# Kernel tuning notes

Hardware: AMD Instinct MI355X
Metric: run time of the kernel (lower is better)

The kernel has to match this reference:

```python
import jax, jax.numpy as jnp
import numpy as np

# ---- HashGrid config (tcnn defaults from module __init__) ----
N_LEVELS = 6
F = 2                      # n_features_per_level
T = 2 ** 19                # hashmap size
BASE = 16                  # base_resolution, per_level_scale=2.0
_RES = [BASE * (2 ** l) for l in range(N_LEVELS)]          # 16..512
_SIZES = [min(r ** 3, T) for r in _RES]                    # dense if grid fits
_OFFSETS = [0] + list(np.cumsum(_SIZES))
TOTAL_ENTRIES = int(_OFFSETS[-1])
_PRIMES = (1, 2654435761, 805459861)
BOX_R = 1.0
DIM_H = 64
DIM_IN = 3 + N_LEVELS * F


def hash_encode(xn, grid):
    """Multi-res hash-grid encoding. xn: [N,3] in [0,1]; grid: [TOTAL_ENTRIES, F]."""
    feats = []
    for l in range(N_LEVELS):
        res, size, off = _RES[l], _SIZES[l], _OFFSETS[l]
        dense = (res ** 3) <= T
        pos = xn * jnp.float32(res - 1) + 0.5          # tcnn: scale*x + 0.5
        pg = jnp.floor(pos)
        frac = pos - pg                                # [N,3]
        pgi = pg.astype(jnp.uint32)
        acc = jnp.zeros((xn.shape[0], F), xn.dtype)
        for corner in range(8):                        # trilinear, 8 corners
            cb = jnp.array([(corner >> d) & 1 for d in range(3)], dtype=jnp.uint32)
            c = pgi + cb                               # [N,3] corner coords
            w = jnp.prod(jnp.where(cb == 1, frac, 1.0 - frac), axis=-1)  # [N]
            if dense:
                c = jnp.minimum(c, jnp.uint32(res - 1))
                idx = c[:, 0] + c[:, 1] * jnp.uint32(res) + c[:, 2] * jnp.uint32(res * res)
            else:
                idx = ((c[:, 0] * jnp.uint32(_PRIMES[0]))
                       ^ (c[:, 1] * jnp.uint32(_PRIMES[1]))
                       ^ (c[:, 2] * jnp.uint32(_PRIMES[2]))) % jnp.uint32(size)
            acc = acc + w[:, None] * grid[jnp.uint32(off) + idx]
        feats.append(acc)
    return jnp.concatenate(feats, axis=-1)             # [N, 12]


def setup_inputs() -> dict:
    key = jax.random.key(0)
    k0, k1, k2 = jax.random.split(key, 3)
    N = 2_097_152
    x = jax.random.uniform(k0, (N, 3), jnp.float32, -1.0, 1.0)
    grid = jax.random.uniform(k1, (TOTAL_ENTRIES, F), jnp.float32, -1e-2, 1e-2)
    W0 = jax.random.normal(k2, (DIM_IN, DIM_H), jnp.float32) * float(np.sqrt(2.0 / DIM_H))
    b0 = jnp.zeros((DIM_H,), jnp.float32)
    W1 = jnp.full((DIM_H, 1), float(np.sqrt(np.pi / DIM_H)), jnp.float32)
    b1 = jnp.full((1,), -1.0, jnp.float32)             # -init_radius
    return {"x": x, "grid": grid, "W0": W0, "b0": b0, "W1": W1, "b1": b1}


def reference(x, grid, W0, b0, W1, b1):
    xn = (x + BOX_R) / (2.0 * BOX_R)                   # normalize to [0,1]
    f = hash_encode(xn, grid)                          # [N,12]
    h = jnp.concatenate([x, f], axis=-1)               # [N,15]
    h = jax.nn.relu(h @ W0 + b0)                       # [N,64]
    return h @ W1 + b1                                 # [N,1] scalar level s
```

## Files before the change

### kernel.cpp

```cpp
#include <hip/hip_runtime.h>


#define HP1 2654435761u
#define HP2 805459861u
#define HMASK ((1u << 19) - 1u)

static __device__ __forceinline__ unsigned umin_(unsigned a, unsigned b) {
    return a < b ? a : b;
}

static __device__ __forceinline__ unsigned f2bf(float f) {
    unsigned u = __float_as_uint(f);
    return (u + 0x7fffu + ((u >> 16) & 1u)) >> 16;
}
static __device__ __forceinline__ float bf2f_lo(unsigned p) {
    return __uint_as_float((p & 0xffffu) << 16);
}
static __device__ __forceinline__ float bf2f_hi(unsigned p) {
    return __uint_as_float(p & 0xffff0000u);
}

__global__ __launch_bounds__(256) void prep_kernel(
    const float* __restrict__ W0, const float* __restrict__ b0,
    const float* __restrict__ W1, const float* __restrict__ b1,
    float* __restrict__ wt)
{
    for (int t = threadIdx.x; t < 1024; t += 256) {
        const int j = t >> 4, i = t & 15;
        wt[t] = (i == 15) ? b0[j] : W0[i * 64 + j];
    }
    if (threadIdx.x < 64) wt[1024 + threadIdx.x] = W1[threadIdx.x];
    if (threadIdx.x == 0) wt[1088] = b1[0];
}

__global__ __launch_bounds__(256) void hash_level_kernel(
    const float* __restrict__ x,
    const float2* __restrict__ tab,
    unsigned* __restrict__ feat,
    float scale, int N)
{
    const int gid = blockIdx.x * 256 + threadIdx.x;
    if (gid >= N) return;

    const float px = __builtin_nontemporal_load(x + 3 * gid + 0);
    const float py = __builtin_nontemporal_load(x + 3 * gid + 1);
    const float pz = __builtin_nontemporal_load(x + 3 * gid + 2);

    const float p0 = fmaf((px + 1.0f) * 0.5f, scale, 0.5f);
    const float p1 = fmaf((py + 1.0f) * 0.5f, scale, 0.5f);
    const float p2 = fmaf((pz + 1.0f) * 0.5f, scale, 0.5f);
    const float g0 = floorf(p0), g1 = floorf(p1), g2 = floorf(p2);
    const float f0 = p0 - g0, f1 = p1 - g1, f2 = p2 - g2;
    const unsigned i0 = (unsigned)g0, i1 = (unsigned)g1, i2 = (unsigned)g2;

    const float wx[2] = {1.0f - f0, f0};
    const float wy[2] = {1.0f - f1, f1};
    const float wz[2] = {1.0f - f2, f2};
    const unsigned hx[2] = {i0, i0 + 1u};
    const unsigned hy[2] = {i1 * HP1, (i1 + 1u) * HP1};
    const unsigned hz[2] = {i2 * HP2, (i2 + 1u) * HP2};

    unsigned idx[8];
    float w[8];
    #pragma unroll
    for (int c = 0; c < 8; ++c) {
        const int bx = c & 1, by = (c >> 1) & 1, bz = (c >> 2) & 1;
        idx[c] = (hx[bx] ^ hy[by] ^ hz[bz]) & HMASK;
        w[c] = wx[bx] * wy[by] * wz[bz];
    }
    float2 v[8];
    #pragma unroll
    for (int c = 0; c < 8; ++c) v[c] = tab[idx[c]];

    float a0 = 0.0f, a1 = 0.0f;
    #pragma unroll
    for (int c = 0; c < 8; ++c) {
        a0 = fmaf(w[c], v[c].x, a0);
        a1 = fmaf(w[c], v[c].y, a1);
    }
    __builtin_nontemporal_store(f2bf(a0) | (f2bf(a1) << 16), feat + gid);
}

static __device__ __forceinline__ void dense_level(
    const float2* __restrict__ tab, unsigned res,
    float xn0, float xn1, float xn2, float& o0, float& o1)
{
    const float scale = (float)(res - 1);
    const float p0 = fmaf(xn0, scale, 0.5f);
    const float p1 = fmaf(xn1, scale, 0.5f);
    const float p2 = fmaf(xn2, scale, 0.5f);
    const float g0 = floorf(p0), g1 = floorf(p1), g2 = floorf(p2);
    const float f0 = p0 - g0, f1 = p1 - g1, f2 = p2 - g2;
    const unsigned i0 = (unsigned)g0, i1 = (unsigned)g1, i2 = (unsigned)g2;

    const unsigned rm1 = res - 1u;
    const unsigned cx[2] = {umin_(i0, rm1), umin_(i0 + 1u, rm1)};
    const unsigned cy[2] = {umin_(i1, rm1) * res, umin_(i1 + 1u, rm1) * res};
    const unsigned cz[2] = {umin_(i2, rm1) * res * res,
                            umin_(i2 + 1u, rm1) * res * res};
    const float wx[2] = {1.0f - f0, f0};
    const float wy[2] = {1.0f - f1, f1};
    const float wz[2] = {1.0f - f2, f2};

    float a0 = 0.0f, a1 = 0.0f;
    #pragma unroll
    for (int c = 0; c < 8; ++c) {
        const int bx = c & 1, by = (c >> 1) & 1, bz = (c >> 2) & 1;
        const unsigned idx = cx[bx] + cy[by] + cz[bz];
        const float w = wx[bx] * wy[by] * wz[bz];
        const float2 v = tab[idx];
        a0 = fmaf(w, v.x, a0);
        a1 = fmaf(w, v.y, a1);
    }
    o0 = a0;
    o1 = a1;
}

__global__ __launch_bounds__(256, 4) void dense_mlp_kernel(
    const float* __restrict__ x,
    const float* __restrict__ grid,
    const unsigned* __restrict__ feat,
    const float* __restrict__ wt,
    float* __restrict__ out, int N)
{
    const int tid = threadIdx.x;
    const int base = blockIdx.x * 1024 + tid;
    const float2* gtab = (const float2*)grid;

    float h[4][16];

    #pragma unroll
    for (int k = 0; k < 4; ++k) {
        const int g = base + 256 * k;
        const int gs = (g < N) ? g : 0;

        const float px = __builtin_nontemporal_load(x + 3 * gs + 0);
        const float py = __builtin_nontemporal_load(x + 3 * gs + 1);
        const float pz = __builtin_nontemporal_load(x + 3 * gs + 2);
        const float xn0 = (px + 1.0f) * 0.5f;
        const float xn1 = (py + 1.0f) * 0.5f;
        const float xn2 = (pz + 1.0f) * 0.5f;

        h[k][0] = px; h[k][1] = py; h[k][2] = pz;
        h[k][15] = 1.0f;

        dense_level(gtab + 0u,     16u, xn0, xn1, xn2, h[k][3], h[k][4]);
        dense_level(gtab + 4096u,  32u, xn0, xn1, xn2, h[k][5], h[k][6]);
        dense_level(gtab + 36864u, 64u, xn0, xn1, xn2, h[k][7], h[k][8]);

        #pragma unroll
        for (int l = 0; l < 3; ++l) {
            const unsigned p = __builtin_nontemporal_load(
                feat + (size_t)l * N + gs);
            h[k][9 + 2 * l]  = bf2f_lo(p);
            h[k][10 + 2 * l] = bf2f_hi(p);
        }
    }

    const float b1v = wt[1088];
    float o[4] = {b1v, b1v, b1v, b1v};

    #pragma unroll 4
    for (int j = 0; j < 64; ++j) {
        float r[16];
        #pragma unroll
        for (int i = 0; i < 16; ++i)
            r[i] = wt[j * 16 + i];
        const float w1j = wt[1024 + j];
        #pragma unroll
        for (int k = 0; k < 4; ++k) {
            float s = 0.0f;
            #pragma unroll
            for (int i = 0; i < 16; ++i)
                s = fmaf(h[k][i], r[i], s);
            s = fmaxf(s, 0.0f);
            o[k] = fmaf(s, w1j, o[k]);
        }
    }

    #pragma unroll
    for (int k = 0; k < 4; ++k) {
        const int g = base + 256 * k;
        if (g < N) __builtin_nontemporal_store(o[k], out + g);
    }
}

extern "C" void kernel_launch(void* const* d_in, const int* in_sizes, int n_in,
                              void* d_out, int out_size, void* d_ws, size_t ws_size,
                              hipStream_t stream) {
    const float* x    = (const float*)d_in[0];
    const float* grid = (const float*)d_in[1];
    const float* W0   = (const float*)d_in[2];
    const float* b0   = (const float*)d_in[3];
    const float* W1   = (const float*)d_in[4];
    const float* b1   = (const float*)d_in[5];
    float* out = (float*)d_out;

    const int N = in_sizes[0] / 3;
    const int blocks1 = (N + 255) / 256;
    const int blocks4 = (N + 1023) / 1024;

    const float2* gtab = (const float2*)grid;
    unsigned* feat = (unsigned*)d_ws;
    const size_t feat_bytes = ((size_t)3 * N * 4 + 255) & ~(size_t)255;
    float* wt = (float*)((char*)d_ws + feat_bytes);

    prep_kernel<<<1, 256, 0, stream>>>(W0, b0, W1, b1, wt);

    hash_level_kernel<<<blocks1, 256, 0, stream>>>(x, gtab + 299008u,
                                                   feat + (size_t)0 * N, 127.0f, N);
    hash_level_kernel<<<blocks1, 256, 0, stream>>>(x, gtab + 823296u,
                                                   feat + (size_t)1 * N, 255.0f, N);
    hash_level_kernel<<<blocks1, 256, 0, stream>>>(x, gtab + 1347584u,
                                                   feat + (size_t)2 * N, 511.0f, N);
    dense_mlp_kernel<<<blocks4, 256, 0, stream>>>(x, grid, feat, wt, out, N);
}
```

Before: 370.9 us.

## Spatially bucket-sort query points before hash-grid gathers to improve locality

Adds a histogram, scan and scatter pass that reorders the input points into 32^3 spatial buckets, then runs the hash and dense-MLP kernels on the sorted points and scatters outputs back through a permutation. The aim is for neighbouring threads to touch nearby grid entries, so the random table gathers hit cache more often. In exchange it adds extra passes over N points, heavy global atomics on the bucket counters, a scattered output write, and it only runs if the workspace is large enough. Spatial hashing at fine levels still scatters nearby corners across the table, so the locality gain may be limited.

```diff
diff --git a/kernel.cpp b/kernel.cpp
--- a/kernel.cpp
+++ b/kernel.cpp
@@ -4,6 +4,7 @@
 #define HP1 2654435761u
 #define HP2 805459861u
 #define HMASK ((1u << 19) - 1u)
+#define NBUCK 32768
 
 static __device__ __forceinline__ unsigned umin_(unsigned a, unsigned b) {
     return a < b ? a : b;
@@ -18,6 +19,16 @@
 }
 static __device__ __forceinline__ float bf2f_hi(unsigned p) {
     return __uint_as_float(p & 0xffff0000u);
+}
+
+static __device__ __forceinline__ unsigned bucket_of(float px, float py, float pz) {
+    const float xn0 = (px + 1.0f) * 0.5f;
+    const float xn1 = (py + 1.0f) * 0.5f;
+    const float xn2 = (pz + 1.0f) * 0.5f;
+    const unsigned qx = umin_((unsigned)(xn0 * 32.0f), 31u);
+    const unsigned qy = umin_((unsigned)(xn1 * 32.0f), 31u);
+    const unsigned qz = umin_((unsigned)(xn2 * 32.0f), 31u);
+    return qz * 1024u + qy * 32u + qx;
 }
 
 __global__ __launch_bounds__(256) void prep_kernel(
@@ -31,6 +42,52 @@
     }
     if (threadIdx.x < 64) wt[1024 + threadIdx.x] = W1[threadIdx.x];
     if (threadIdx.x == 0) wt[1088] = b1[0];
+}
+
+__global__ __launch_bounds__(256) void hist_kernel(
+    const float* __restrict__ x, unsigned* __restrict__ hist, int N)
+{
+    const int g = blockIdx.x * 256 + threadIdx.x;
+    if (g >= N) return;
+    const unsigned b = bucket_of(x[3 * g], x[3 * g + 1], x[3 * g + 2]);
+    atomicAdd(&hist[b], 1u);
+}
+
+__global__ __launch_bounds__(256) void scan_kernel(unsigned* __restrict__ hist)
+{
+    __shared__ unsigned ssum[256];
+    const int t = threadIdx.x;
+    constexpr int CH = NBUCK / 256;
+    unsigned s = 0;
+    for (int i = 0; i < CH; ++i) s += hist[t * CH + i];
+    ssum[t] = s;
+    __syncthreads();
+    if (t == 0) {
+        unsigned run = 0;
+        for (int i = 0; i < 256; ++i) { unsigned v = ssum[i]; ssum[i] = run; run += v; }
+    }
+    __syncthreads();
+    unsigned run = ssum[t];
+    for (int i = 0; i < CH; ++i) {
+        const unsigned v = hist[t * CH + i];
+        hist[t * CH + i] = run;
+        run += v;
+    }
+}
+
+__global__ __launch_bounds__(256) void scatter_kernel(
+    const float* __restrict__ x, unsigned* __restrict__ cursor,
+    float* __restrict__ sx, unsigned* __restrict__ perm, int N)
+{
+    const int g = blockIdx.x * 256 + threadIdx.x;
+    if (g >= N) return;
+    const float px = x[3 * g], py = x[3 * g + 1], pz = x[3 * g + 2];
+    const unsigned b = bucket_of(px, py, pz);
+    const unsigned pos = atomicAdd(&cursor[b], 1u);
+    __builtin_nontemporal_store(px, sx + 3 * pos + 0);
+    __builtin_nontemporal_store(py, sx + 3 * pos + 1);
+    __builtin_nontemporal_store(pz, sx + 3 * pos + 2);
+    __builtin_nontemporal_store((unsigned)g, perm + pos);
 }
 
 __global__ __launch_bounds__(256) void hash_level_kernel(
@@ -121,6 +178,7 @@
     const float* __restrict__ grid,
     const unsigned* __restrict__ feat,
     const float* __restrict__ wt,
+    const unsigned* __restrict__ perm,
     float* __restrict__ out, int N)
 {
     const int tid = threadIdx.x;
@@ -181,7 +239,10 @@
     #pragma unroll
     for (int k = 0; k < 4; ++k) {
         const int g = base + 256 * k;
-        if (g < N) __builtin_nontemporal_store(o[k], out + g);
+        if (g < N) {
+            const int d = perm ? (int)perm[g] : g;
+            __builtin_nontemporal_store(o[k], out + d);
+        }
     }
 }
 
@@ -201,17 +262,41 @@
     const int blocks4 = (N + 1023) / 1024;
 
     const float2* gtab = (const float2*)grid;
-    unsigned* feat = (unsigned*)d_ws;
-    const size_t feat_bytes = ((size_t)3 * N * 4 + 255) & ~(size_t)255;
-    float* wt = (float*)((char*)d_ws + feat_bytes);
+
+    auto align256 = [](size_t v) { return (v + 255) & ~(size_t)255; };
+    size_t off = 0;
+    const size_t feat_off = off; off += align256((size_t)3 * N * 4);
+    const size_t wt_off   = off; off += align256(1089 * 4);
+    const size_t sx_off   = off; off += align256((size_t)3 * N * 4);
+    const size_t perm_off = off; off += align256((size_t)N * 4);
+    const size_t hist_off = off; off += align256(NBUCK * 4);
+    const bool do_sort = (ws_size >= off);
+
+    unsigned* feat = (unsigned*)((char*)d_ws + feat_off);
+    float*    wt   = (float*)((char*)d_ws + wt_off);
+    float*    sx   = (float*)((char*)d_ws + sx_off);
+    unsigned* perm = (unsigned*)((char*)d_ws + perm_off);
+    unsigned* hist = (unsigned*)((char*)d_ws + hist_off);
 
     prep_kernel<<<1, 256, 0, stream>>>(W0, b0, W1, b1, wt);
 
-    hash_level_kernel<<<blocks1, 256, 0, stream>>>(x, gtab + 299008u,
+    const float* px = x;
+    const unsigned* pperm = nullptr;
+    if (do_sort) {
+        hipMemsetAsync(hist, 0, NBUCK * 4, stream);
+        hist_kernel<<<blocks1, 256, 0, stream>>>(x, hist, N);
+        scan_kernel<<<1, 256, 0, stream>>>(hist);
+        scatter_kernel<<<blocks1, 256, 0, stream>>>(x, hist, sx, perm, N);
+        px = sx;
+        pperm = perm;
+    }
+
+    hash_level_kernel<<<blocks1, 256, 0, stream>>>(px, gtab + 299008u,
                                                    feat + (size_t)0 * N, 127.0f, N);
-    hash_level_kernel<<<blocks1, 256, 0, stream>>>(x, gtab + 823296u,
+    hash_level_kernel<<<blocks1, 256, 0, stream>>>(px, gtab + 823296u,
                                                    feat + (size_t)1 * N, 255.0f, N);
-    hash_level_kernel<<<blocks1, 256, 0, stream>>>(x, gtab + 1347584u,
+    hash_level_kernel<<<blocks1, 256, 0, stream>>>(px, gtab + 1347584u,
                                                    feat + (size_t)2 * N, 511.0f, N);
-    dense_mlp_kernel<<<blocks4, 256, 0, stream>>>(x, grid, feat, wt, out, N);
-}
+    dense_mlp_kernel<<<blocks4, 256, 0, stream>>>(px, grid, feat, wt, pperm,
+                                                  out, N);
+}
```

Measured after the change: 599.1 us. 61.5% more time.

## Stage bf16-packed dense grid levels in LDS for the dense MLP kernel

Applied to the files above, without the earlier changes.

A wider prep kernel now packs the first two dense grid levels (36864 entries) into bf16 pairs in workspace. The dense+MLP kernel becomes a template that copies this packed table into shared memory before doing its trilinear lookups. When the device allows 144KB of dynamic LDS, it runs with 1024-thread blocks and both levels 0 and 1 in LDS. Otherwise it uses 256-thread blocks with only level 0 in LDS. This swaps global or L2 gathers for LDS reads, but every block now pays a large up-front copy, occupancy drops to about one block per CU, and the dense-level features lose precision to bf16.

```diff
diff --git a/kernel.cpp b/kernel.cpp
--- a/kernel.cpp
+++ b/kernel.cpp
@@ -23,14 +23,22 @@
 __global__ __launch_bounds__(256) void prep_kernel(
     const float* __restrict__ W0, const float* __restrict__ b0,
     const float* __restrict__ W1, const float* __restrict__ b1,
-    float* __restrict__ wt)
-{
-    for (int t = threadIdx.x; t < 1024; t += 256) {
-        const int j = t >> 4, i = t & 15;
-        wt[t] = (i == 15) ? b0[j] : W0[i * 64 + j];
-    }
-    if (threadIdx.x < 64) wt[1024 + threadIdx.x] = W1[threadIdx.x];
-    if (threadIdx.x == 0) wt[1088] = b1[0];
+    const float2* __restrict__ gtab,
+    float* __restrict__ wt, unsigned* __restrict__ packed)
+{
+    for (int t = blockIdx.x * 256 + threadIdx.x; t < 36864;
+         t += gridDim.x * 256) {
+        const float2 e = gtab[t];
+        packed[t] = f2bf(e.x) | (f2bf(e.y) << 16);
+    }
+    if (blockIdx.x == 0) {
+        for (int t = threadIdx.x; t < 1024; t += 256) {
+            const int j = t >> 4, i = t & 15;
+            wt[t] = (i == 15) ? b0[j] : W0[i * 64 + j];
+        }
+        if (threadIdx.x < 64) wt[1024 + threadIdx.x] = W1[threadIdx.x];
+        if (threadIdx.x == 0) wt[1088] = b1[0];
+    }
 }
 
 __global__ __launch_bounds__(256) void hash_level_kernel(
@@ -116,22 +124,65 @@
     o1 = a1;
 }
 
-__global__ __launch_bounds__(256, 4) void dense_mlp_kernel(
+static __device__ __forceinline__ void dense_level_lds(
+    const unsigned* __restrict__ sPk, unsigned off, unsigned res,
+    float xn0, float xn1, float xn2, float& o0, float& o1)
+{
+    const float scale = (float)(res - 1);
+    const float p0 = fmaf(xn0, scale, 0.5f);
+    const float p1 = fmaf(xn1, scale, 0.5f);
+    const float p2 = fmaf(xn2, scale, 0.5f);
+    const float g0 = floorf(p0), g1 = floorf(p1), g2 = floorf(p2);
+    const float f0 = p0 - g0, f1 = p1 - g1, f2 = p2 - g2;
+    const unsigned i0 = (unsigned)g0, i1 = (unsigned)g1, i2 = (unsigned)g2;
+
+    const unsigned rm1 = res - 1u;
+    const unsigned cx[2] = {umin_(i0, rm1), umin_(i0 + 1u, rm1)};
+    const unsigned cy[2] = {umin_(i1, rm1) * res, umin_(i1 + 1u, rm1) * res};
+    const unsigned cz[2] = {umin_(i2, rm1) * res * res,
+                            umin_(i2 + 1u, rm1) * res * res};
+    const float wx[2] = {1.0f - f0, f0};
+    const float wy[2] = {1.0f - f1, f1};
+    const float wz[2] = {1.0f - f2, f2};
+
+    float a0 = 0.0f, a1 = 0.0f;
+    #pragma unroll
+    for (int c = 0; c < 8; ++c) {
+        const int bx = c & 1, by = (c >> 1) & 1, bz = (c >> 2) & 1;
+        const unsigned p = sPk[off + cx[bx] + cy[by] + cz[bz]];
+        const float w = wx[bx] * wy[by] * wz[bz];
+        a0 = fmaf(w, bf2f_lo(p), a0);
+        a1 = fmaf(w, bf2f_hi(p), a1);
+    }
+    o0 = a0;
+    o1 = a1;
+}
+
+template<int BLOCK, bool L1LDS>
+__global__ __launch_bounds__(BLOCK, 4) void dense_mlp_kernel(
     const float* __restrict__ x,
     const float* __restrict__ grid,
     const unsigned* __restrict__ feat,
     const float* __restrict__ wt,
+    const unsigned* __restrict__ packed,
     float* __restrict__ out, int N)
 {
+    extern __shared__ unsigned sPk[];
     const int tid = threadIdx.x;
-    const int base = blockIdx.x * 1024 + tid;
+
+    const int nstage = L1LDS ? 36864 : 4096;
+    for (int t = tid; t < nstage; t += BLOCK)
+        sPk[t] = packed[t];
+    __syncthreads();
+
+    const int base = blockIdx.x * (BLOCK * 4) + tid;
     const float2* gtab = (const float2*)grid;
 
     float h[4][16];
 
     #pragma unroll
     for (int k = 0; k < 4; ++k) {
-        const int g = base + 256 * k;
+        const int g = base + BLOCK * k;
         const int gs = (g < N) ? g : 0;
 
         const float px = __builtin_nontemporal_load(x + 3 * gs + 0);
@@ -144,8 +195,11 @@
         h[k][0] = px; h[k][1] = py; h[k][2] = pz;
         h[k][15] = 1.0f;
 
-        dense_level(gtab + 0u,     16u, xn0, xn1, xn2, h[k][3], h[k][4]);
-        dense_level(gtab + 4096u,  32u, xn0, xn1, xn2, h[k][5], h[k][6]);
+        dense_level_lds(sPk, 0u, 16u, xn0, xn1, xn2, h[k][3], h[k][4]);
+        if (L1LDS)
+            dense_level_lds(sPk, 4096u, 32u, xn0, xn1, xn2, h[k][5], h[k][6]);
+        else
+            dense_level(gtab + 4096u, 32u, xn0, xn1, xn2, h[k][5], h[k][6]);
         dense_level(gtab + 36864u, 64u, xn0, xn1, xn2, h[k][7], h[k][8]);
 
         #pragma unroll
@@ -180,7 +234,7 @@
 
     #pragma unroll
     for (int k = 0; k < 4; ++k) {
-        const int g = base + 256 * k;
+        const int g = base + BLOCK * k;
         if (g < N) __builtin_nontemporal_store(o[k], out + g);
     }
 }
@@ -198,14 +252,21 @@
 
     const int N = in_sizes[0] / 3;
     const int blocks1 = (N + 255) / 256;
-    const int blocks4 = (N + 1023) / 1024;
 
     const float2* gtab = (const float2*)grid;
-    unsigned* feat = (unsigned*)d_ws;
-    const size_t feat_bytes = ((size_t)3 * N * 4 + 255) & ~(size_t)255;
-    float* wt = (float*)((char*)d_ws + feat_bytes);
-
-    prep_kernel<<<1, 256, 0, stream>>>(W0, b0, W1, b1, wt);
+
+    auto align256 = [](size_t v) { return (v + 255) & ~(size_t)255; };
+    size_t off = 0;
+    const size_t feat_off = off; off += align256((size_t)3 * N * 4);
+    const size_t wt_off   = off; off += align256(1089 * 4);
+    const size_t pk_off   = off; off += align256(36864 * 4);
+    (void)ws_size;
+
+    unsigned* feat   = (unsigned*)((char*)d_ws + feat_off);
+    float*    wt     = (float*)((char*)d_ws + wt_off);
+    unsigned* packed = (unsigned*)((char*)d_ws + pk_off);
+
+    prep_kernel<<<64, 256, 0, stream>>>(W0, b0, W1, b1, gtab, wt, packed);
 
     hash_level_kernel<<<blocks1, 256, 0, stream>>>(x, gtab + 299008u,
                                                    feat + (size_t)0 * N, 127.0f, N);
@@ -213,5 +274,24 @@
                                                    feat + (size_t)1 * N, 255.0f, N);
     hash_level_kernel<<<blocks1, 256, 0, stream>>>(x, gtab + 1347584u,
                                                    feat + (size_t)2 * N, 511.0f, N);
-    dense_mlp_kernel<<<blocks4, 256, 0, stream>>>(x, grid, feat, wt, out, N);
-}
+
+    const size_t bigShm = 36864u * 4u;
+    const void* bigK =
+        reinterpret_cast<const void*>(&dense_mlp_kernel<1024, true>);
+    (void)hipFuncSetAttribute(bigK,
+        hipFuncAttributeMaxDynamicSharedMemorySize, (int)bigShm);
+    bool big = false;
+    hipFuncAttributes fa{};
+    if (hipFuncGetAttributes(&fa, bigK) == hipSuccess)
+        big = ((size_t)fa.maxDynamicSharedSizeBytes >= bigShm);
+
+    if (big) {
+        const int blocksB = (N + 4095) / 4096;
+        dense_mlp_kernel<1024, true><<<blocksB, 1024, bigShm, stream>>>(
+            x, (const float*)grid, feat, wt, packed, out, N);
+    } else {
+        const int blocksF = (N + 1023) / 1024;
+        dense_mlp_kernel<256, false><<<blocksF, 256, 4096u * 4u, stream>>>(
+            x, (const float*)grid, feat, wt, packed, out, N);
+    }
+}
```

Measured after the change: 335.1 us. -9.7%, faster.
